# Performance work log

Hardware: AMD Instinct MI355X
Metric: run time of the kernel (lower is better)

## Reference

```python
import jax, jax.numpy as jnp
import numpy as np

K = 9   # kernel_size (neighbors)
D = 1   # dilation


def setup_inputs() -> dict:
    key = jax.random.key(0)
    k1, k2 = jax.random.split(key)
    B, C, N, OUT = 8, 64, 4096, 128
    x = jax.random.normal(k1, (B, C, N), dtype=jnp.float32)
    W = jax.random.normal(k2, (OUT, 2 * C), dtype=jnp.float32) * 0.05
    b = jnp.zeros((OUT,), dtype=jnp.float32)
    return {"x": x, "W": W, "b": b}


def dilated_knn(x, k, d):
    # x: [B, C, N] -> nn_idx: [B, N, k] (indices of k nearest neighbors, dilated)
    x = jax.lax.stop_gradient(x)  # original detaches x for graph construction
    x2 = jnp.sum(x * x, axis=1)                      # [B, N]
    inner = jnp.einsum('bcn,bcm->bnm', x, x)         # [B, N, N]
    neg_dist = 2.0 * inner - x2[:, :, None] - x2[:, None, :]  # -||xi-xj||^2
    _, idx = jax.lax.top_k(neg_dist, k * d)          # [B, N, k*d]
    return idx[..., ::d]                             # dilated selection -> [B, N, k]


def reference(x, W, b):
    # x: [B, C, N]
    nn_idx = dilated_knn(x, K, D)                    # [B, N, k]
    # gather neighbor features: x_j[b, c, n, kk] = x[b, c, nn_idx[b, n, kk]]
    x_j = jax.vmap(lambda xb, ib: xb[:, ib])(x, nn_idx)  # [B, C, N, k]
    # max-relative: max_k (x_j - x_i)
    x_max = jnp.max(x_j - x[:, :, :, None], axis=-1)     # [B, C, N]
    h = jnp.concatenate([x, x_max], axis=1)              # [B, 2C, N]
    # 1x1 conv + bias + ReLU
    out = jnp.einsum('oc,bcn->bon', W, h) + b[None, :, None]
    return jax.nn.relu(out)
```

## Files before the change

kernel.cpp:

```cpp
#include <hip/hip_runtime.h>
#include <float.h>

#define B_   8
#define C_   64
#define N_   4096
#define OUT_ 128
#define KNN  9
#define CAP  64
#define TAU_A 2.15f

typedef __attribute__((ext_vector_type(8))) short short8;
typedef __attribute__((ext_vector_type(4))) float f32x4;

__device__ inline unsigned short f2bf(float f) {
    unsigned u = __float_as_uint(f);
    unsigned r = (u + 0x7fffu + ((u >> 16) & 1u)) >> 16;
    return (unsigned short)r;
}
__device__ inline float bf2f(unsigned short s) {
    return __uint_as_float(((unsigned)s) << 16);
}


__global__ void k_wt(const float* __restrict__ W, unsigned short* __restrict__ wfrag) {
    int mt = blockIdx.x, kc = threadIdx.x >> 6, L = threadIdx.x & 63;
    int o  = mt * 16 + (L & 15);
    int c0 = kc * 32 + ((L >> 4) * 8);
    const float* src = W + (size_t)o * 128 + c0;
    float4 v0 = *(const float4*)src, v1 = *(const float4*)(src + 4);
    float vs[8] = {v0.x, v0.y, v0.z, v0.w, v1.x, v1.y, v1.z, v1.w};
    short8 hi, lo;
#pragma unroll
    for (int j = 0; j < 8; ++j) {
        unsigned short hb = f2bf(vs[j]);
        float hf = bf2f(hb);
        lo[j] = (short)f2bf(vs[j] - hf);
        hi[j] = (short)hb;
    }
    size_t cb = (size_t)(mt * 4 + kc) * 2 * 512;
    *(short8*)(wfrag + cb + L * 8)       = hi;
    *(short8*)(wfrag + cb + 512 + L * 8) = lo;
}

__global__ void k_transpose(const float* __restrict__ x, float* __restrict__ xT,
                            float* __restrict__ x2, unsigned short* __restrict__ xfrag) {
    __shared__ float t[C_][65];
    int b  = blockIdx.x & 7;
    int n0 = (blockIdx.x >> 3) * 64;
    int tid = threadIdx.x;
    for (int i = 0; i < 16; ++i) {
        int e = i * 256 + tid;
        int c = e >> 6, nn = e & 63;
        t[c][nn] = x[((size_t)b * C_ + c) * N_ + n0 + nn];
    }
    __syncthreads();
    for (int i = 0; i < 16; ++i) {
        int e = i * 256 + tid;
        int nn = e >> 6, c = e & 63;
        xT[((size_t)b * N_ + n0 + nn) * C_ + c] = t[c][nn];
    }
    int q = tid >> 6, L = tid & 63;
    int mloc = q * 16 + (L & 15);
    int k8 = (L >> 4) * 8;
    size_t cb = (size_t)(b * 256 + (n0 >> 4) + q) * 2 * 512;
#pragma unroll
    for (int h = 0; h < 2; ++h) {
        short8 hi;
#pragma unroll
        for (int j = 0; j < 8; ++j)
            hi[j] = (short)f2bf(t[h * 32 + k8 + j][mloc]);
        *(short8*)(xfrag + cb + h * 512 + L * 8) = hi;
    }
    if (tid < 64) {
        float s = 0.f;
        for (int c = 0; c < C_; ++c) { float v = t[c][tid]; s += v * v; }
        x2[(size_t)b * N_ + n0 + tid] = s;
    }
}

#define APPEND(KEY, TAU, LN, MIDX)                                      \
    if ((KEY) > (TAU)) {                                                \
        unsigned u = __float_as_uint(KEY);                              \
        u = (u & 0x80000000u) ? ~u : (u | 0x80000000u);                 \
        unsigned pk = (u & 0xFFFFF000u) | (unsigned)(MIDX);             \
        int sl = atomicAdd(&cnt_s[LN], 1);                              \
        if (sl < CAP) buf_s[LN][sl] = pk;                               \
    }

__global__ __launch_bounds__(512, 4) void k_topk_mf(const unsigned short* __restrict__ xfrag,
                                                    const float* __restrict__ x2,
                                                    unsigned* __restrict__ cand24,
                                                    int* __restrict__ cnt2) {
    __shared__ int cnt_s[64];
    __shared__ unsigned buf_s[64][CAP];
    int b    = blockIdx.x & 7;
    int mh   = (blockIdx.x >> 3) & 1;
    int ng   = blockIdx.x >> 4;
    int wave = threadIdx.x >> 6, lane = threadIdx.x & 63;
    if (threadIdx.x < 64) cnt_s[threadIdx.x] = 0;

    const short8* fr = (const short8*)xfrag;

    short8 Bh[4][2];
#pragma unroll
    for (int q = 0; q < 4; ++q)
#pragma unroll
        for (int h = 0; h < 2; ++h) {
            int ch = ((b * 256 + ng * 4 + q) * 2 + h);
            Bh[q][h] = fr[(size_t)ch * 64 + lane];
        }

    float tau[4];
#pragma unroll
    for (int q = 0; q < 4; ++q) {
        float x2n = x2[b * N_ + ng * 64 + q * 16 + (lane & 15)];
        tau[q] = TAU_A * sqrtf(fmaf(4.f, x2n, 128.f)) - 64.f;
    }

    int mt0 = mh * 128 + wave * 16;
    const short8* pA = fr + (size_t)(b * 256 + mt0) * 2 * 64 + lane;
    const f32x4*  px2 = (const f32x4*)(x2 + b * N_ + mt0 * 16 + (lane >> 4) * 4);
    short8 Ah0 = pA[0], Ah1 = pA[64];
    f32x4 x2v = *px2;

    __syncthreads();

    for (int i = 0; i < 16; ++i) {
        if (i != 15) { pA += 128; px2 += 4; }
        short8 nAh0 = pA[0], nAh1 = pA[64];
        f32x4 nx2 = *px2;

        int mbase = (mt0 + i) * 16 + (lane >> 4) * 4;

#pragma unroll
        for (int q = 0; q < 4; ++q) {
            f32x4 acc = {0.f, 0.f, 0.f, 0.f};
            acc = __builtin_amdgcn_mfma_f32_16x16x32_bf16(Ah0, Bh[q][0], acc, 0, 0, 0);
            acc = __builtin_amdgcn_mfma_f32_16x16x32_bf16(Ah1, Bh[q][1], acc, 0, 0, 0);
            float k0 = fmaf(2.f, acc[0], -x2v[0]);
            float k1 = fmaf(2.f, acc[1], -x2v[1]);
            float k2 = fmaf(2.f, acc[2], -x2v[2]);
            float k3 = fmaf(2.f, acc[3], -x2v[3]);
            float kmax = fmaxf(fmaxf(k0, k1), fmaxf(k2, k3));
            if (kmax > tau[q]) {
                int ln = q * 16 + (lane & 15);
                APPEND(k0, tau[q], ln, mbase + 0)
                APPEND(k1, tau[q], ln, mbase + 1)
                APPEND(k2, tau[q], ln, mbase + 2)
                APPEND(k3, tau[q], ln, mbase + 3)
            }
        }
        Ah0 = nAh0; Ah1 = nAh1; x2v = nx2;
    }

    __syncthreads();
    if (threadIdx.x < 64) {
        int r = threadIdx.x;
        int c = cnt_s[r];
        size_t grow = (size_t)b * N_ + ng * 64 + r;
        cnt2[grow * 2 + mh] = c;
        int cc = min(c, CAP);
        unsigned best[12];
#pragma unroll
        for (int j = 0; j < 12; ++j) best[j] = 0u;
        for (int s = 0; s < cc; ++s) {
            unsigned v = buf_s[r][s];
            if (v > best[0]) {
                best[0] = v;
#pragma unroll
                for (int j = 0; j < 11; ++j) {
                    bool sw = best[j] > best[j + 1];
                    unsigned t = best[j];
                    best[j]     = sw ? best[j + 1] : best[j];
                    best[j + 1] = sw ? t : best[j + 1];
                }
            }
        }
#pragma unroll
        for (int j = 0; j < 12; ++j)
            cand24[grow * 24 + mh * 12 + j] = best[11 - j];
    }
}

__global__ void k_refine(const float* __restrict__ xT, const unsigned* __restrict__ cand24,
                         const int* __restrict__ cnt2, int* __restrict__ idx9) {
    int wave = threadIdx.x >> 6, lane = threadIdx.x & 63;
    int half = lane >> 5, hl = lane & 31;
    int b = blockIdx.x & 7;
    int row = b * N_ + (blockIdx.x >> 3) * 8 + wave * 2 + half;
    int c0 = cnt2[(size_t)row * 2 + 0];
    int c1 = cnt2[(size_t)row * 2 + 1];
    bool ok = (c0 + c1 >= KNN) && (c0 <= CAP) && (c1 <= CAP);
    int c0c = min(c0, 12), c1c = min(c1, 12);

    double mykey = -1e300; int myidx = 0x7fffffff;
    bool valid = ok && ((hl < 12) ? (hl < c0c) : (hl < 24 && (hl - 12) < c1c));
    if (valid) {
        int m = (int)(cand24[(size_t)row * 24 + hl] & 0xFFFu);
        const float* xi = xT + (size_t)row * C_;
        const float* xm = xT + (((size_t)b << 12) + m) * C_;
        double d = 0.0, s2 = 0.0;
#pragma unroll
        for (int c4 = 0; c4 < 16; ++c4) {
            float4 a = *(const float4*)(xi + c4 * 4);
            float4 v = *(const float4*)(xm + c4 * 4);
            d = fma((double)a.x, (double)v.x, d);  s2 = fma((double)v.x, (double)v.x, s2);
            d = fma((double)a.y, (double)v.y, d);  s2 = fma((double)v.y, (double)v.y, s2);
            d = fma((double)a.z, (double)v.z, d);  s2 = fma((double)v.z, (double)v.z, s2);
            d = fma((double)a.w, (double)v.w, d);  s2 = fma((double)v.w, (double)v.w, s2);
        }
        mykey = 2.0 * d - s2;
        myidx = m;
    }
    for (int r = 0; r < KNN; ++r) {
        double k = mykey; int ix = myidx;
#pragma unroll
        for (int o = 16; o; o >>= 1) {
            double ok2 = __shfl_xor(k, o); int oi = __shfl_xor(ix, o);
            bool take = (ok2 > k) || (ok2 == k && oi < ix);
            k = take ? ok2 : k; ix = take ? oi : ix;
        }
        if (ok && hl == 0) idx9[(size_t)row * KNN + r] = ix;
        if (myidx == ix) { mykey = -1e300; myidx = 0x7fffffff; }
    }
}

__global__ void k_fallback(const float* __restrict__ xT, const int* __restrict__ cnt2,
                           int* __restrict__ idx9) {
    int wave = threadIdx.x >> 6, lane = threadIdx.x & 63;
    int row = blockIdx.x * 4 + wave;
    int c0 = cnt2[(size_t)row * 2 + 0];
    int c1 = cnt2[(size_t)row * 2 + 1];
    if ((c0 + c1 >= KNN) && (c0 <= CAP) && (c1 <= CAP)) return;
    int b = row >> 12;
    const float* xi = xT + (size_t)row * C_;
    float4 xr[16];
#pragma unroll
    for (int c4 = 0; c4 < 16; ++c4) xr[c4] = *(const float4*)(xi + c4 * 4);
    double sk[9]; int si[9];
#pragma unroll
    for (int j = 0; j < 9; ++j) { sk[j] = -1e300; si[j] = 0x7fffffff; }
    for (int mb = 0; mb < N_; mb += 64) {
        int m = mb + lane;
        const float* xm = xT + (((size_t)b << 12) + m) * C_;
        double d0 = 0.0, d1 = 0.0, s0 = 0.0, s1 = 0.0;
#pragma unroll
        for (int c4 = 0; c4 < 16; c4 += 2) {
            float4 v = *(const float4*)(xm + c4 * 4);
            float4 w = *(const float4*)(xm + c4 * 4 + 4);
            float4 a = xr[c4], bb = xr[c4 + 1];
            d0 = fma((double)a.x, (double)v.x, d0);  s0 = fma((double)v.x, (double)v.x, s0);
            d0 = fma((double)a.y, (double)v.y, d0);  s0 = fma((double)v.y, (double)v.y, s0);
            d0 = fma((double)a.z, (double)v.z, d0);  s0 = fma((double)v.z, (double)v.z, s0);
            d0 = fma((double)a.w, (double)v.w, d0);  s0 = fma((double)v.w, (double)v.w, s0);
            d1 = fma((double)bb.x, (double)w.x, d1); s1 = fma((double)w.x, (double)w.x, s1);
            d1 = fma((double)bb.y, (double)w.y, d1); s1 = fma((double)w.y, (double)w.y, s1);
            d1 = fma((double)bb.z, (double)w.z, d1); s1 = fma((double)w.z, (double)w.z, s1);
            d1 = fma((double)bb.w, (double)w.w, d1); s1 = fma((double)w.w, (double)w.w, s1);
        }
        double key = 2.0 * (d0 + d1) - (s0 + s1);
        if (key > sk[0] || (key == sk[0] && m < si[0])) {
            sk[0] = key; si[0] = m;
#pragma unroll
            for (int j = 0; j < 8; ++j) {
                bool sw = (sk[j] > sk[j + 1]) || (sk[j] == sk[j + 1] && si[j] < si[j + 1]);
                double tk = sk[j]; int ti = si[j];
                sk[j]     = sw ? sk[j + 1] : sk[j];
                si[j]     = sw ? si[j + 1] : si[j];
                sk[j + 1] = sw ? tk : sk[j + 1];
                si[j + 1] = sw ? ti : si[j + 1];
            }
        }
    }
    for (int r = 0; r < KNN; ++r) {
        double k = sk[8]; int ix = si[8];
#pragma unroll
        for (int o = 32; o; o >>= 1) {
            double ok = __shfl_xor(k, o); int oi = __shfl_xor(ix, o);
            bool take = (ok > k) || (ok == k && oi < ix);
            k = take ? ok : k; ix = take ? oi : ix;
        }
        if (lane == 0) idx9[(size_t)row * KNN + r] = ix;
        if (si[8] == ix) {
#pragma unroll
            for (int j = 8; j > 0; --j) { sk[j] = sk[j - 1]; si[j] = si[j - 1]; }
            sk[0] = -1e300; si[0] = 0x7fffffff;
        }
    }
}

__global__ __launch_bounds__(256, 2) void k_gemm(const float* __restrict__ xT,
                                                 const int* __restrict__ idx9,
                                                 const unsigned short* __restrict__ wfrag,
                                                 const float* __restrict__ bias,
                                                 float* __restrict__ out) {
    __shared__ float h[128][65];
    int b  = blockIdx.x & 7;
    int n0 = (blockIdx.x >> 3) * 64;
    int wave = threadIdx.x >> 6, lane = threadIdx.x & 63;

    const short8* fw = (const short8*)wfrag;
    short8 Wh[2][4], Wl[2][4];
#pragma unroll
    for (int t = 0; t < 2; ++t)
#pragma unroll
        for (int kc = 0; kc < 4; ++kc) {
            size_t cb = (size_t)((wave * 2 + t) * 4 + kc) * 2 * 64;
            Wh[t][kc] = fw[cb + lane];
            Wl[t][kc] = fw[cb + 64 + lane];
        }

    for (int r = 0; r < 16; ++r) {
        int nn = wave * 16 + r;
        size_t row = (size_t)b * N_ + n0 + nn;
        const int* id = idx9 + row * KNN;
        float m = -FLT_MAX;
#pragma unroll
        for (int k = 0; k < KNN; ++k) {
            int j = id[k];
            m = fmaxf(m, xT[(((size_t)b << 12) + j) * C_ + lane]);
        }
        float xic = xT[row * C_ + lane];
        h[lane][nn]      = xic;
        h[64 + lane][nn] = m - xic;
    }
    __syncthreads();

    f32x4 acc[2][4];
#pragma unroll
    for (int t = 0; t < 2; ++t)
#pragma unroll
        for (int nt = 0; nt < 4; ++nt) acc[t][nt] = (f32x4){0.f, 0.f, 0.f, 0.f};

    int cb0 = (lane >> 4) * 8;
    int nl  = lane & 15;
#pragma unroll
    for (int kc = 0; kc < 4; ++kc) {
#pragma unroll
        for (int nt = 0; nt < 4; ++nt) {
            short8 bh, bl;
#pragma unroll
            for (int j = 0; j < 8; ++j) {
                float v = h[kc * 32 + cb0 + j][nt * 16 + nl];
                unsigned short hb = f2bf(v);
                bl[j] = (short)f2bf(v - bf2f(hb));
                bh[j] = (short)hb;
            }
#pragma unroll
            for (int t = 0; t < 2; ++t) {
                acc[t][nt] = __builtin_amdgcn_mfma_f32_16x16x32_bf16(Wh[t][kc], bh, acc[t][nt], 0, 0, 0);
                acc[t][nt] = __builtin_amdgcn_mfma_f32_16x16x32_bf16(Wl[t][kc], bh, acc[t][nt], 0, 0, 0);
                acc[t][nt] = __builtin_amdgcn_mfma_f32_16x16x32_bf16(Wh[t][kc], bl, acc[t][nt], 0, 0, 0);
            }
        }
    }
    __syncthreads();

    f32x4 bs[2];
#pragma unroll
    for (int t = 0; t < 2; ++t)
        bs[t] = *(const f32x4*)(bias + wave * 32 + t * 16 + (lane >> 4) * 4);
#pragma unroll
    for (int t = 0; t < 2; ++t)
#pragma unroll
        for (int nt = 0; nt < 4; ++nt)
#pragma unroll
            for (int j = 0; j < 4; ++j) {
                float v = acc[t][nt][j] + bs[t][j];
                h[wave * 32 + t * 16 + (lane >> 4) * 4 + j][nt * 16 + nl] = fmaxf(v, 0.f);
            }
    __syncthreads();

#pragma unroll
    for (int rr = 0; rr < 32; ++rr) {
        int o = wave * 32 + rr;
        out[((size_t)b * OUT_ + o) * N_ + n0 + lane] = h[o][lane];
    }
}

extern "C" void kernel_launch(void* const* d_in, const int* in_sizes, int n_in,
                              void* d_out, int out_size, void* d_ws, size_t ws_size,
                              hipStream_t stream) {
    const float* x    = (const float*)d_in[0];
    const float* W    = (const float*)d_in[1];
    const float* bias = (const float*)d_in[2];
    float* out = (float*)d_out;
    char* ws = (char*)d_ws;

    float*          xT     = (float*)(ws);
    unsigned short* xfrag  = (unsigned short*)(ws + 8388608);
    int*            idx9   = (int*)(ws + 8388608);
    float*          x2     = (float*)(ws + 16777216);
    unsigned short* wfrag  = (unsigned short*)(ws + 16908288);
    unsigned*       cand24 = (unsigned*)(ws + 16973824);
    int*            cnt2   = (int*)(ws + 20119552);

    k_wt       <<<dim3(8),    dim3(256), 0, stream>>>(W, wfrag);
    k_transpose<<<dim3(512),  dim3(256), 0, stream>>>(x, xT, x2, xfrag);
    k_topk_mf  <<<dim3(1024), dim3(512), 0, stream>>>(xfrag, x2, cand24, cnt2);
    k_refine   <<<dim3(4096), dim3(256), 0, stream>>>(xT, cand24, cnt2, idx9);
    k_fallback <<<dim3(8192), dim3(256), 0, stream>>>(xT, cnt2, idx9);
    k_gemm     <<<dim3(512),  dim3(256), 0, stream>>>(xT, idx9, wfrag, bias, out);
}
```

Baseline: 119.6 us.

## Deepen top-k prefetch to two tiles and stage refine candidates through LDS

The top-k MFMA loop now prefetches A fragments and x2 two tiles ahead instead of one, to hide more global load latency. The refine kernel uses one wave per row instead of half a wave. Each wave loads the up-to-24 candidate feature rows into LDS with coalesced float4 loads, so each lane no longer does its own scattered strided reads. The grid doubles and the argmax reduction widens to 64 lanes. The cost is more LDS per block, more blocks, and one extra prefetch read past the end of the last tile.

```diff
diff --git a/kernel.cpp b/kernel.cpp
--- a/kernel.cpp
+++ b/kernel.cpp
@@ -85,6 +85,26 @@
         unsigned pk = (u & 0xFFFFF000u) | (unsigned)(MIDX);             \
         int sl = atomicAdd(&cnt_s[LN], 1);                              \
         if (sl < CAP) buf_s[LN][sl] = pk;                               \
+    }
+
+#define TILE_COMPUTE(AH0, AH1, X2V, MBASE)                              \
+    _Pragma("unroll")                                                   \
+    for (int q = 0; q < 4; ++q) {                                       \
+        f32x4 acc = {0.f, 0.f, 0.f, 0.f};                               \
+        acc = __builtin_amdgcn_mfma_f32_16x16x32_bf16(AH0, Bh[q][0], acc, 0, 0, 0); \
+        acc = __builtin_amdgcn_mfma_f32_16x16x32_bf16(AH1, Bh[q][1], acc, 0, 0, 0); \
+        float k0 = fmaf(2.f, acc[0], -(X2V)[0]);                        \
+        float k1 = fmaf(2.f, acc[1], -(X2V)[1]);                        \
+        float k2 = fmaf(2.f, acc[2], -(X2V)[2]);                        \
+        float k3 = fmaf(2.f, acc[3], -(X2V)[3]);                        \
+        float kmax = fmaxf(fmaxf(k0, k1), fmaxf(k2, k3));               \
+        if (kmax > tau[q]) {                                            \
+            int ln = q * 16 + (lane & 15);                              \
+            APPEND(k0, tau[q], ln, (MBASE) + 0)                         \
+            APPEND(k1, tau[q], ln, (MBASE) + 1)                         \
+            APPEND(k2, tau[q], ln, (MBASE) + 2)                         \
+            APPEND(k3, tau[q], ln, (MBASE) + 3)                         \
+        }                                                               \
     }
 
 __global__ __launch_bounds__(512, 4) void k_topk_mf(const unsigned short* __restrict__ xfrag,
@@ -120,37 +140,25 @@
     int mt0 = mh * 128 + wave * 16;
     const short8* pA = fr + (size_t)(b * 256 + mt0) * 2 * 64 + lane;
     const f32x4*  px2 = (const f32x4*)(x2 + b * N_ + mt0 * 16 + (lane >> 4) * 4);
-    short8 Ah0 = pA[0], Ah1 = pA[64];
-    f32x4 x2v = *px2;
+
+    short8 Ph0 = pA[0], Ph1 = pA[64];
+    f32x4  xp  = px2[0];
+    pA += 128; px2 += 4;
+    short8 Qh0 = pA[0], Qh1 = pA[64];
+    f32x4  xq  = px2[0];
 
     __syncthreads();
 
     for (int i = 0; i < 16; ++i) {
-        if (i != 15) { pA += 128; px2 += 4; }
-        short8 nAh0 = pA[0], nAh1 = pA[64];
-        f32x4 nx2 = *px2;
+        pA += 128; px2 += 4;
+        short8 Rh0 = pA[0], Rh1 = pA[64];
+        f32x4  xr  = px2[0];
 
         int mbase = (mt0 + i) * 16 + (lane >> 4) * 4;
-
-#pragma unroll
-        for (int q = 0; q < 4; ++q) {
-            f32x4 acc = {0.f, 0.f, 0.f, 0.f};
-            acc = __builtin_amdgcn_mfma_f32_16x16x32_bf16(Ah0, Bh[q][0], acc, 0, 0, 0);
-            acc = __builtin_amdgcn_mfma_f32_16x16x32_bf16(Ah1, Bh[q][1], acc, 0, 0, 0);
-            float k0 = fmaf(2.f, acc[0], -x2v[0]);
-            float k1 = fmaf(2.f, acc[1], -x2v[1]);
-            float k2 = fmaf(2.f, acc[2], -x2v[2]);
-            float k3 = fmaf(2.f, acc[3], -x2v[3]);
-            float kmax = fmaxf(fmaxf(k0, k1), fmaxf(k2, k3));
-            if (kmax > tau[q]) {
-                int ln = q * 16 + (lane & 15);
-                APPEND(k0, tau[q], ln, mbase + 0)
-                APPEND(k1, tau[q], ln, mbase + 1)
-                APPEND(k2, tau[q], ln, mbase + 2)
-                APPEND(k3, tau[q], ln, mbase + 3)
-            }
-        }
-        Ah0 = nAh0; Ah1 = nAh1; x2v = nx2;
+        TILE_COMPUTE(Ph0, Ph1, xp, mbase)
+
+        Ph0 = Qh0; Ph1 = Qh1; xp = xq;
+        Qh0 = Rh0; Qh1 = Rh1; xq = xr;
     }
 
     __syncthreads();
@@ -182,28 +190,42 @@
     }
 }
 
-__global__ void k_refine(const float* __restrict__ xT, const unsigned* __restrict__ cand24,
-                         const int* __restrict__ cnt2, int* __restrict__ idx9) {
+__global__ __launch_bounds__(256) void k_refine(const float* __restrict__ xT,
+                                                const unsigned* __restrict__ cand24,
+                                                const int* __restrict__ cnt2,
+                                                int* __restrict__ idx9) {
+    __shared__ float rs[4][24][67];
     int wave = threadIdx.x >> 6, lane = threadIdx.x & 63;
-    int half = lane >> 5, hl = lane & 31;
     int b = blockIdx.x & 7;
-    int row = b * N_ + (blockIdx.x >> 3) * 8 + wave * 2 + half;
+    int row = b * N_ + (blockIdx.x >> 3) * 4 + wave;
     int c0 = cnt2[(size_t)row * 2 + 0];
     int c1 = cnt2[(size_t)row * 2 + 1];
     bool ok = (c0 + c1 >= KNN) && (c0 <= CAP) && (c1 <= CAP);
     int c0c = min(c0, 12), c1c = min(c1, 12);
 
+    int g = lane >> 4, s = lane & 15;
+#pragma unroll
+    for (int cc = 0; cc < 6; ++cc) {
+        int cj = cc * 4 + g;
+        bool v = ok && ((cj < 12) ? (cj < c0c) : ((cj - 12) < c1c));
+        if (v) {
+            int m = (int)(cand24[(size_t)row * 24 + cj] & 0xFFFu);
+            float4 t = *(const float4*)(xT + (((size_t)b << 12) + m) * C_ + s * 4);
+            *(float4*)&rs[wave][cj][s * 4] = t;
+        }
+    }
+
+    int j = lane;
+    bool jvalid = ok && (j < 24) && ((j < 12) ? (j < c0c) : ((j - 12) < c1c));
     double mykey = -1e300; int myidx = 0x7fffffff;
-    bool valid = ok && ((hl < 12) ? (hl < c0c) : (hl < 24 && (hl - 12) < c1c));
-    if (valid) {
-        int m = (int)(cand24[(size_t)row * 24 + hl] & 0xFFFu);
+    if (jvalid) {
+        int m = (int)(cand24[(size_t)row * 24 + j] & 0xFFFu);
         const float* xi = xT + (size_t)row * C_;
-        const float* xm = xT + (((size_t)b << 12) + m) * C_;
         double d = 0.0, s2 = 0.0;
 #pragma unroll
         for (int c4 = 0; c4 < 16; ++c4) {
             float4 a = *(const float4*)(xi + c4 * 4);
-            float4 v = *(const float4*)(xm + c4 * 4);
+            float4 v = *(const float4*)&rs[wave][j][c4 * 4];
             d = fma((double)a.x, (double)v.x, d);  s2 = fma((double)v.x, (double)v.x, s2);
             d = fma((double)a.y, (double)v.y, d);  s2 = fma((double)v.y, (double)v.y, s2);
             d = fma((double)a.z, (double)v.z, d);  s2 = fma((double)v.z, (double)v.z, s2);
@@ -215,12 +237,12 @@
     for (int r = 0; r < KNN; ++r) {
         double k = mykey; int ix = myidx;
 #pragma unroll
-        for (int o = 16; o; o >>= 1) {
+        for (int o = 32; o; o >>= 1) {
             double ok2 = __shfl_xor(k, o); int oi = __shfl_xor(ix, o);
             bool take = (ok2 > k) || (ok2 == k && oi < ix);
             k = take ? ok2 : k; ix = take ? oi : ix;
         }
-        if (ok && hl == 0) idx9[(size_t)row * KNN + r] = ix;
+        if (ok && lane == 0) idx9[(size_t)row * KNN + r] = ix;
         if (myidx == ix) { mykey = -1e300; myidx = 0x7fffffff; }
     }
 }
@@ -398,7 +420,7 @@
     k_wt       <<<dim3(8),    dim3(256), 0, stream>>>(W, wfrag);
     k_transpose<<<dim3(512),  dim3(256), 0, stream>>>(x, xT, x2, xfrag);
     k_topk_mf  <<<dim3(1024), dim3(512), 0, stream>>>(xfrag, x2, cand24, cnt2);
-    k_refine   <<<dim3(4096), dim3(256), 0, stream>>>(xT, cand24, cnt2, idx9);
+    k_refine   <<<dim3(8192), dim3(256), 0, stream>>>(xT, cand24, cnt2, idx9);
     k_fallback <<<dim3(8192), dim3(256), 0, stream>>>(xT, cnt2, idx9);
     k_gemm     <<<dim3(512),  dim3(256), 0, stream>>>(xT, idx9, wfrag, bias, out);
 }
```

After: 155.3 us. 1.3x slower.
